# Performance work log

Measured on AMD Instinct MI355X. Metric: run time of the kernel, lower is better.

Reference implementation:

```python
import jax, jax.numpy as jnp
import numpy as np

B = 1024      # number of subgraphs in the batch
S = 128       # nodes per subgraph (last node is the anchor)
N = B * S     # total nodes
E = 2_097_152 # total edges (avg degree 16)
F_IN = 300
F_OUT = 64


def setup_inputs() -> dict:
    key = jax.random.key(0)
    kx, kg, ks, kd, kw = jax.random.split(key, 5)
    in_feat = jax.random.normal(kx, (N, F_IN), dtype=jnp.float32)
    # edges constrained within subgraphs (batched DGL graph semantics)
    gid = jax.random.randint(kg, (E,), 0, B)
    src = (gid * S + jax.random.randint(ks, (E,), 0, S)).astype(jnp.int32)
    dst = (gid * S + jax.random.randint(kd, (E,), 0, S)).astype(jnp.int32)
    W = jax.random.normal(kw, (F_IN, F_OUT), dtype=jnp.float32) * 0.05
    b = jnp.zeros((F_OUT,), dtype=jnp.float32)
    prelu_a = jnp.float32(0.25)  # nn.PReLU default single parameter
    return {"in_feat": in_feat, "W": W, "b": b, "prelu_a": prelu_a,
            "src": src, "dst": dst}


def reference(in_feat, W, b, prelu_a, src, dst):
    ones = jnp.ones((E,), dtype=jnp.float32)
    deg_out = jnp.clip(jax.ops.segment_sum(ones, src, num_segments=N), 1.0)
    deg_in = jnp.clip(jax.ops.segment_sum(ones, dst, num_segments=N), 1.0)
    # GraphConv norm='both': weight first (in_feats > out_feats), then SpMM
    x = in_feat * jax.lax.rsqrt(deg_out)[:, None]
    h = x @ W                                   # [N, F_OUT]
    agg = jax.ops.segment_sum(h[src], dst, num_segments=N)
    h = agg * jax.lax.rsqrt(deg_in)[:, None] + b
    # PReLU
    h = jnp.where(h > 0, h, prelu_a * h)
    # ragged per-subgraph mean over all nodes except the last (anchor)
    node_idx = jnp.arange(N)
    seg = node_idx // S                          # subgraph id per node
    not_anchor = ((node_idx % S) != (S - 1)).astype(h.dtype)
    pool_sum = jax.ops.segment_sum(h * not_anchor[:, None], seg, num_segments=B)
    subgraph_pool_emb = pool_sum / jnp.float32(S - 1)
    anchor_out = h[(jnp.arange(B) + 1) * S - 1]  # last node of each subgraph
    return subgraph_pool_emb, anchor_out
```

## Files before the change

### kernel.cpp

```cpp
#include <hip/hip_runtime.h>
#include <hip/hip_bf16.h>

#define NNODES 131072
#define NEDGES 2097152
#define BSUB   1024
#define SSUB   128
#define FIN    300
#define FOUT   64
#define NCHUNK 256
#define CHEDGE 8192

typedef __attribute__((ext_vector_type(8))) short short8;
typedef __attribute__((ext_vector_type(8))) unsigned short ushort8;
typedef __attribute__((ext_vector_type(4))) float f32x4;

__device__ inline unsigned short f2bfbits(float f) {
    union { __hip_bfloat16 h; unsigned short u; } cv;
    cv.h = __float2bfloat16(f);
    return cv.u;
}
__device__ inline float bf2f(unsigned short b) {
    return __uint_as_float(((unsigned)b) << 16);
}

__device__ inline void gload_lds16(const float* g, void* l) {
    __builtin_amdgcn_global_load_lds(
        (const __attribute__((address_space(1))) unsigned int*)g,
        (__attribute__((address_space(3))) unsigned int*)l,
        16, 0, 0);
}

__global__ __launch_bounds__(256) void prep_w_kernel(const float* __restrict__ W,
                                                     short* __restrict__ wfrag) {
    int idx = blockIdx.x * 256 + threadIdx.x;
    if (idx >= 2560) return;
    int ct   = idx / 640;
    int rem  = idx % 640;
    int kt   = rem / 64;
    int lane = rem % 64;
    int col  = ct * 16 + (lane & 15);
    int kb   = kt * 32 + (lane >> 4) * 8;
#pragma unroll
    for (int e = 0; e < 8; ++e) {
        int k = kb + e;
        float v = (k < FIN) ? W[(size_t)k * FOUT + col] : 0.f;
        wfrag[(size_t)idx * 8 + e] = (short)f2bfbits(v);
    }
}

__global__ __launch_bounds__(256) void bucket_kernel(const int* __restrict__ src,
                                                     const int* __restrict__ dst,
                                                     unsigned* __restrict__ ofs,
                                                     unsigned short* __restrict__ bkt) {
    __shared__ unsigned short epack[CHEDGE];
    __shared__ unsigned short eg[CHEDGE];
    __shared__ unsigned short sorted[CHEDGE];
    __shared__ int hist[BSUB];
    __shared__ int cur[BSUB];
    __shared__ int wsum[4];

    const int cb = blockIdx.x;
    const int t = threadIdx.x;
    for (int i = t; i < BSUB; i += 256) hist[i] = 0;
    __syncthreads();

    const int4* sp = (const int4*)(src + (size_t)cb * CHEDGE);
    const int4* dp = (const int4*)(dst + (size_t)cb * CHEDGE);
    for (int i = t; i < CHEDGE / 4; i += 256) {
        int4 s4 = sp[i], d4 = dp[i];
#pragma unroll
        for (int k = 0; k < 4; ++k) {
            int s = (k == 0) ? s4.x : (k == 1) ? s4.y : (k == 2) ? s4.z : s4.w;
            int d = (k == 0) ? d4.x : (k == 1) ? d4.y : (k == 2) ? d4.z : d4.w;
            int g = s >> 7;
            epack[i * 4 + k] = (unsigned short)(((s & 127) << 7) | (d & 127));
            eg[i * 4 + k] = (unsigned short)g;
            atomicAdd(&hist[g], 1);
        }
    }
    __syncthreads();

    {
        int lane = t & 63, w = t >> 6;
        int c0 = hist[4 * t], c1 = hist[4 * t + 1], c2 = hist[4 * t + 2], c3 = hist[4 * t + 3];
        int s = c0 + c1 + c2 + c3;
        int pre = s;
#pragma unroll
        for (int o = 1; o < 64; o <<= 1) {
            int v = __shfl_up(pre, o, 64);
            if (lane >= o) pre += v;
        }
        if (lane == 63) wsum[w] = pre;
        __syncthreads();
        int wbase = 0;
        for (int i = 0; i < w; ++i) wbase += wsum[i];
        int excl = wbase + pre - s;
        uint4 ov;
        ov.x = ((unsigned)excl << 16) | (unsigned)c0; cur[4 * t]     = excl; excl += c0;
        ov.y = ((unsigned)excl << 16) | (unsigned)c1; cur[4 * t + 1] = excl; excl += c1;
        ov.z = ((unsigned)excl << 16) | (unsigned)c2; cur[4 * t + 2] = excl; excl += c2;
        ov.w = ((unsigned)excl << 16) | (unsigned)c3; cur[4 * t + 3] = excl;
        ((uint4*)(ofs + (size_t)cb * BSUB))[t] = ov;
    }
    __syncthreads();

    for (int i = t; i < CHEDGE; i += 256) {
        int g = eg[i];
        int r = atomicAdd(&cur[g], 1);
        sorted[r] = epack[i];
    }
    __syncthreads();

    {
        ushort8* outv = (ushort8*)(bkt + (size_t)cb * CHEDGE);
        const ushort8* sv = (const ushort8*)sorted;
        for (int i = t; i < CHEDGE / 8; i += 256) outv[i] = sv[i];
    }
}

__global__ __launch_bounds__(256, 2) void gemm_kernel(const float* __restrict__ x,
                                                      const short* __restrict__ wfrag,
                                                      unsigned short* __restrict__ hb) {
    __shared__ __align__(16) char smem[77824];
    char* bufA = smem;
    char* bufB = smem + 32768;
    char* aux  = smem + 65536;

    const int wave = threadIdx.x >> 6;
    const int lane = threadIdx.x & 63;
    const int rowbase = blockIdx.x * 64;

    short8 bq[10];
#pragma unroll
    for (int kt = 0; kt < 10; ++kt)
        bq[kt] = *(const short8*)(wfrag + ((size_t)(wave * 10 + kt) * 64 + lane) * 8);

#pragma unroll
    for (int i = wave; i < 32; i += 4) {
        int o = i * 1024 + lane * 16;
        int row = o >> 9;
        int c = o & 511;
        int csrc = c ^ ((row & 7) << 4);
        gload_lds16(x + (size_t)(rowbase + row) * FIN + (csrc >> 2), bufA + i * 1024);
    }
#pragma unroll
    for (int i = wave; i < 32; i += 4) {
        int o = i * 1024 + lane * 16;
        int row = o >> 9;
        int c = o & 511;
        int csrc = c ^ ((row & 7) << 4);
        gload_lds16(x + (size_t)(rowbase + row) * FIN + 128 + (csrc >> 2), bufB + i * 1024);
    }
    for (int i = wave; i < 11; i += 4) {
        int o = i * 1024 + lane * 16;
        int row = o / 176;
        int c = o - row * 176;
        gload_lds16(x + (size_t)(rowbase + row) * FIN + 256 + (c >> 2), aux + i * 1024);
    }
    ((float*)(aux + 11264))[threadIdx.x] = 0.f;

    f32x4 acc[4];
#pragma unroll
    for (int r = 0; r < 4; ++r) acc[r] = (f32x4){0.f, 0.f, 0.f, 0.f};

    const int kg = lane >> 4;

    __syncthreads();

#pragma unroll
    for (int rt = 0; rt < 4; ++rt) {
        const int rl = rt * 16 + (lane & 15);
        const int sw = (rl & 7) << 4;
#pragma unroll
        for (int kt = 0; kt < 10; ++kt) {
            f32x4 lo, hi;
            if (kt < 8) {
                const char* buf = (kt < 4) ? bufA : bufB;
                int c0 = (kt & 3) * 128 + kg * 32;
                lo = *(const f32x4*)(buf + rl * 512 + (c0 ^ sw));
                hi = *(const f32x4*)(buf + rl * 512 + ((c0 + 16) ^ sw));
            } else {
                int c0 = (kt - 8) * 128 + kg * 32;
                lo = *(const f32x4*)(aux + rl * 176 + c0);
                hi = *(const f32x4*)(aux + rl * 176 + c0 + 16);
            }
            short8 afr;
            afr[0] = (short)f2bfbits(lo[0]); afr[1] = (short)f2bfbits(lo[1]);
            afr[2] = (short)f2bfbits(lo[2]); afr[3] = (short)f2bfbits(lo[3]);
            afr[4] = (short)f2bfbits(hi[0]); afr[5] = (short)f2bfbits(hi[1]);
            afr[6] = (short)f2bfbits(hi[2]); afr[7] = (short)f2bfbits(hi[3]);
            acc[rt] = __builtin_amdgcn_mfma_f32_16x16x32_bf16(afr, bq[kt], acc[rt], 0, 0, 0);
        }
    }

    __syncthreads();

    {
        unsigned short* st = (unsigned short*)aux;
        const int colb = wave * 16 + (lane & 15);
#pragma unroll
        for (int rt = 0; rt < 4; ++rt) {
            const int rbase = rt * 16 + (lane >> 4) * 4;
#pragma unroll
            for (int r = 0; r < 4; ++r)
                st[(rbase + r) * FOUT + colb] = f2bfbits(acc[rt][r]);
        }
        __syncthreads();
        const ushort8* sv = (const ushort8*)st;
        ushort8* hout = (ushort8*)(hb + (size_t)rowbase * FOUT);
        hout[threadIdx.x] = sv[threadIdx.x];
        hout[threadIdx.x + 256] = sv[threadIdx.x + 256];
    }
}

__global__ __launch_bounds__(256) void agg_pool_kernel(const unsigned short* __restrict__ hb,
                                                       const unsigned short* __restrict__ bkt,
                                                       const unsigned* __restrict__ ofs,
                                                       const float* __restrict__ bias,
                                                       const float* __restrict__ prelu,
                                                       float* __restrict__ out) {
    __shared__ unsigned short hl[SSUB][FOUT];
    __shared__ unsigned char  es[SSUB][64];
    __shared__ int   din[SSUB];
    __shared__ int   dout[SSUB];
    __shared__ float rout[SSUB];
    __shared__ float ps[4][FOUT];

    const int g = blockIdx.x;
    const int t = threadIdx.x;
    const int lane = t & 63;
    const int w = t >> 6;

    {
        const ushort8* hsrc = (const ushort8*)(hb + (size_t)g * SSUB * FOUT);
        ushort8* hdst = (ushort8*)&hl[0][0];
        for (int i = t; i < 1024; i += 256) hdst[i] = hsrc[i];
    }
    if (t < SSUB) { din[t] = 0; dout[t] = 0; }
    __syncthreads();

    {
        unsigned w32 = ofs[(size_t)t * BSUB + g];
        int st = (int)(w32 >> 16), cn = (int)(w32 & 0xffff);
        const unsigned short* ebb = bkt + ((size_t)t << 13) + st;
        for (int i = 0; i < cn; ++i) {
            unsigned e = ebb[i];
            int s = e >> 7, d = e & 127;
            int r = atomicAdd(&din[d], 1);
            es[d][r & 63] = (unsigned char)s;
            atomicAdd(&dout[s], 1);
        }
    }
    __syncthreads();
    if (t < SSUB) rout[t] = rsqrtf((float)max(dout[t], 1));
    __syncthreads();

    const float bv = bias[lane];
    const float a = prelu[0];
    float pool = 0.f;
#pragma unroll 4
    for (int ii = 0; ii < 32; ++ii) {
        int d = w + 4 * ii;
        int cd = min(din[d], 64);
        float accv = 0.f;
        const unsigned* ew = (const unsigned*)&es[d][0];
        int nw = (cd + 3) >> 2;
        for (int p = 0; p < nw; ++p) {
            unsigned wd = ew[p];
            int rem = cd - p * 4;
#pragma unroll
            for (int b = 0; b < 4; ++b) {
                if (b < rem) {
                    int s = (wd >> (8 * b)) & 127;
                    accv += bf2f(hl[s][lane]) * rout[s];
                }
            }
        }
        float v = accv * rsqrtf((float)max(din[d], 1)) + bv;
        v = (v > 0.f) ? v : a * v;
        if (d == SSUB - 1)
            out[(size_t)(BSUB + g) * FOUT + lane] = v;
        else
            pool += v;
    }
    ps[w][lane] = pool;
    __syncthreads();
    if (w == 0) {
        float s = (ps[0][lane] + ps[1][lane]) + (ps[2][lane] + ps[3][lane]);
        out[(size_t)g * FOUT + lane] = s * (1.0f / 127.0f);
    }
}

extern "C" void kernel_launch(void* const* d_in, const int* in_sizes, int n_in,
                              void* d_out, int out_size, void* d_ws, size_t ws_size,
                              hipStream_t stream) {
    const float* in_feat = (const float*)d_in[0];
    const float* W       = (const float*)d_in[1];
    const float* bias    = (const float*)d_in[2];
    const float* prelu   = (const float*)d_in[3];
    const int*   src     = (const int*)d_in[4];
    const int*   dst     = (const int*)d_in[5];
    float* out = (float*)d_out;

    char* ws = (char*)d_ws;
    short*          wfrag = (short*)(ws + 65536);
    unsigned*       ofs   = (unsigned*)(ws + (2u << 20));
    unsigned short* bkt   = (unsigned short*)(ws + (4u << 20));
    unsigned short* hb    = (unsigned short*)(ws + (16u << 20));

    hipLaunchKernelGGL(prep_w_kernel,   dim3(10),        dim3(256), 0, stream, W, wfrag);
    hipLaunchKernelGGL(bucket_kernel,   dim3(NCHUNK),    dim3(256), 0, stream, src, dst, ofs, bkt);
    hipLaunchKernelGGL(gemm_kernel,     dim3(NNODES/64), dim3(256), 0, stream, in_feat, wfrag, hb);
    hipLaunchKernelGGL(agg_pool_kernel, dim3(BSUB),      dim3(256), 0, stream, hb, bkt, ofs, bias, prelu, out);
}
```

Measured before the change: 108.0 us.

## Fuse GEMM into per-subgraph aggregation kernel and drop W prep kernel

Merges the dense projection into the aggregation/pooling kernel so each block computes h for its 128 nodes directly into LDS. This removes the bf16 h round-trip through global memory and two kernel launches. W fragments are built per block straight from global memory, and the K tail is loaded into registers instead of LDS. The trade-off is a grid of only 1024 blocks doing the GEMM, which leaves less parallelism and latency hiding than the earlier 2048-block GEMM. Each block also repeats the W conversion.

```diff
diff --git a/kernel.cpp b/kernel.cpp
--- a/kernel.cpp
+++ b/kernel.cpp
@@ -22,30 +22,11 @@
 __device__ inline float bf2f(unsigned short b) {
     return __uint_as_float(((unsigned)b) << 16);
 }
-
 __device__ inline void gload_lds16(const float* g, void* l) {
     __builtin_amdgcn_global_load_lds(
         (const __attribute__((address_space(1))) unsigned int*)g,
         (__attribute__((address_space(3))) unsigned int*)l,
         16, 0, 0);
-}
-
-__global__ __launch_bounds__(256) void prep_w_kernel(const float* __restrict__ W,
-                                                     short* __restrict__ wfrag) {
-    int idx = blockIdx.x * 256 + threadIdx.x;
-    if (idx >= 2560) return;
-    int ct   = idx / 640;
-    int rem  = idx % 640;
-    int kt   = rem / 64;
-    int lane = rem % 64;
-    int col  = ct * 16 + (lane & 15);
-    int kb   = kt * 32 + (lane >> 4) * 8;
-#pragma unroll
-    for (int e = 0; e < 8; ++e) {
-        int k = kb + e;
-        float v = (k < FIN) ? W[(size_t)k * FOUT + col] : 0.f;
-        wfrag[(size_t)idx * 8 + e] = (short)f2bfbits(v);
-    }
 }
 
 __global__ __launch_bounds__(256) void bucket_kernel(const int* __restrict__ src,
@@ -118,126 +99,139 @@
     }
 }
 
-__global__ __launch_bounds__(256, 2) void gemm_kernel(const float* __restrict__ x,
-                                                      const short* __restrict__ wfrag,
-                                                      unsigned short* __restrict__ hb) {
-    __shared__ __align__(16) char smem[77824];
-    char* bufA = smem;
-    char* bufB = smem + 32768;
-    char* aux  = smem + 65536;
-
-    const int wave = threadIdx.x >> 6;
-    const int lane = threadIdx.x & 63;
-    const int rowbase = blockIdx.x * 64;
-
-    short8 bq[10];
-#pragma unroll
-    for (int kt = 0; kt < 10; ++kt)
-        bq[kt] = *(const short8*)(wfrag + ((size_t)(wave * 10 + kt) * 64 + lane) * 8);
-
-#pragma unroll
-    for (int i = wave; i < 32; i += 4) {
-        int o = i * 1024 + lane * 16;
-        int row = o >> 9;
-        int c = o & 511;
-        int csrc = c ^ ((row & 7) << 4);
-        gload_lds16(x + (size_t)(rowbase + row) * FIN + (csrc >> 2), bufA + i * 1024);
-    }
-#pragma unroll
-    for (int i = wave; i < 32; i += 4) {
-        int o = i * 1024 + lane * 16;
-        int row = o >> 9;
-        int c = o & 511;
-        int csrc = c ^ ((row & 7) << 4);
-        gload_lds16(x + (size_t)(rowbase + row) * FIN + 128 + (csrc >> 2), bufB + i * 1024);
-    }
-    for (int i = wave; i < 11; i += 4) {
-        int o = i * 1024 + lane * 16;
-        int row = o / 176;
-        int c = o - row * 176;
-        gload_lds16(x + (size_t)(rowbase + row) * FIN + 256 + (c >> 2), aux + i * 1024);
-    }
-    ((float*)(aux + 11264))[threadIdx.x] = 0.f;
-
-    f32x4 acc[4];
-#pragma unroll
-    for (int r = 0; r < 4; ++r) acc[r] = (f32x4){0.f, 0.f, 0.f, 0.f};
-
-    const int kg = lane >> 4;
-
-    __syncthreads();
-
-#pragma unroll
-    for (int rt = 0; rt < 4; ++rt) {
-        const int rl = rt * 16 + (lane & 15);
-        const int sw = (rl & 7) << 4;
-#pragma unroll
-        for (int kt = 0; kt < 10; ++kt) {
-            f32x4 lo, hi;
-            if (kt < 8) {
-                const char* buf = (kt < 4) ? bufA : bufB;
-                int c0 = (kt & 3) * 128 + kg * 32;
-                lo = *(const f32x4*)(buf + rl * 512 + (c0 ^ sw));
-                hi = *(const f32x4*)(buf + rl * 512 + ((c0 + 16) ^ sw));
-            } else {
-                int c0 = (kt - 8) * 128 + kg * 32;
-                lo = *(const f32x4*)(aux + rl * 176 + c0);
-                hi = *(const f32x4*)(aux + rl * 176 + c0 + 16);
-            }
-            short8 afr;
-            afr[0] = (short)f2bfbits(lo[0]); afr[1] = (short)f2bfbits(lo[1]);
-            afr[2] = (short)f2bfbits(lo[2]); afr[3] = (short)f2bfbits(lo[3]);
-            afr[4] = (short)f2bfbits(hi[0]); afr[5] = (short)f2bfbits(hi[1]);
-            afr[6] = (short)f2bfbits(hi[2]); afr[7] = (short)f2bfbits(hi[3]);
-            acc[rt] = __builtin_amdgcn_mfma_f32_16x16x32_bf16(afr, bq[kt], acc[rt], 0, 0, 0);
-        }
-    }
-
-    __syncthreads();
-
-    {
-        unsigned short* st = (unsigned short*)aux;
-        const int colb = wave * 16 + (lane & 15);
-#pragma unroll
-        for (int rt = 0; rt < 4; ++rt) {
-            const int rbase = rt * 16 + (lane >> 4) * 4;
-#pragma unroll
-            for (int r = 0; r < 4; ++r)
-                st[(rbase + r) * FOUT + colb] = f2bfbits(acc[rt][r]);
-        }
-        __syncthreads();
-        const ushort8* sv = (const ushort8*)st;
-        ushort8* hout = (ushort8*)(hb + (size_t)rowbase * FOUT);
-        hout[threadIdx.x] = sv[threadIdx.x];
-        hout[threadIdx.x + 256] = sv[threadIdx.x + 256];
-    }
-}
-
-__global__ __launch_bounds__(256) void agg_pool_kernel(const unsigned short* __restrict__ hb,
+__global__ __launch_bounds__(256, 2) void fused_kernel(const float* __restrict__ x,
+                                                       const float* __restrict__ W,
                                                        const unsigned short* __restrict__ bkt,
                                                        const unsigned* __restrict__ ofs,
                                                        const float* __restrict__ bias,
                                                        const float* __restrict__ prelu,
                                                        float* __restrict__ out) {
-    __shared__ unsigned short hl[SSUB][FOUT];
-    __shared__ unsigned char  es[SSUB][64];
-    __shared__ int   din[SSUB];
-    __shared__ int   dout[SSUB];
-    __shared__ float rout[SSUB];
-    __shared__ float ps[4][FOUT];
+    __shared__ __align__(16) char smem[59904];
+    char*           buf  = smem;
+    unsigned short* hl   = (unsigned short*)(smem + 32768);
+    unsigned char*  es   = (unsigned char*)(smem + 49152);
+    int*            din  = (int*)(smem + 57344);
+    int*            dout = (int*)(smem + 57856);
+    float*          rout = (float*)(smem + 58368);
+    float*          ps   = (float*)(smem + 58880);
 
     const int g = blockIdx.x;
     const int t = threadIdx.x;
     const int lane = t & 63;
-    const int w = t >> 6;
-
+    const int wave = t >> 6;
+    const int kg = lane >> 4;
+
+    short8 bq[10];
     {
-        const ushort8* hsrc = (const ushort8*)(hb + (size_t)g * SSUB * FOUT);
-        ushort8* hdst = (ushort8*)&hl[0][0];
-        for (int i = t; i < 1024; i += 256) hdst[i] = hsrc[i];
+        const int colW = wave * 16 + (lane & 15);
+        const int krow = kg * 8;
+#pragma unroll
+        for (int kt = 0; kt < 10; ++kt) {
+#pragma unroll
+            for (int e = 0; e < 8; ++e) {
+                int k = kt * 32 + krow + e;
+                float v = (k < FIN) ? W[(size_t)k * FOUT + colW] : 0.f;
+                bq[kt][e] = (short)f2bfbits(v);
+            }
+        }
     }
     if (t < SSUB) { din[t] = 0; dout[t] = 0; }
-    __syncthreads();
+
+#pragma unroll
+    for (int half = 0; half < 2; ++half) {
+        const int rowbase = g * SSUB + half * 64;
+
+        f32x4 t8l[4], t8h[4], t9l[4], t9h[4];
+#pragma unroll
+        for (int rt = 0; rt < 4; ++rt) {
+            const float* arp = x + (size_t)(rowbase + rt * 16 + (lane & 15)) * FIN;
+            t8l[rt] = *(const f32x4*)(arp + 256 + kg * 8);
+            t8h[rt] = *(const f32x4*)(arp + 256 + kg * 8 + 4);
+            t9l[rt] = (f32x4){0.f, 0.f, 0.f, 0.f};
+            t9h[rt] = (f32x4){0.f, 0.f, 0.f, 0.f};
+            if (kg == 0) {
+                t9l[rt] = *(const f32x4*)(arp + 288);
+                t9h[rt] = *(const f32x4*)(arp + 292);
+            } else if (kg == 1) {
+                t9l[rt] = *(const f32x4*)(arp + 296);
+            }
+        }
+
+#pragma unroll
+        for (int i = wave; i < 32; i += 4) {
+            int o = i * 1024 + lane * 16;
+            int row = o >> 9;
+            int c = o & 511;
+            int csrc = c ^ ((row & 7) << 4);
+            gload_lds16(x + (size_t)(rowbase + row) * FIN + (csrc >> 2), buf + i * 1024);
+        }
+
+        f32x4 acc[4];
+#pragma unroll
+        for (int r = 0; r < 4; ++r) acc[r] = (f32x4){0.f, 0.f, 0.f, 0.f};
+
+        __syncthreads();
+
+#pragma unroll
+        for (int rt = 0; rt < 4; ++rt) {
+            const int rl = rt * 16 + (lane & 15);
+            const int sw = (rl & 7) << 4;
+#pragma unroll
+            for (int kt = 0; kt < 4; ++kt) {
+                int c0 = kt * 128 + kg * 32;
+                f32x4 lo = *(const f32x4*)(buf + rl * 512 + (c0 ^ sw));
+                f32x4 hi = *(const f32x4*)(buf + rl * 512 + ((c0 + 16) ^ sw));
+                short8 afr;
+                afr[0] = (short)f2bfbits(lo[0]); afr[1] = (short)f2bfbits(lo[1]);
+                afr[2] = (short)f2bfbits(lo[2]); afr[3] = (short)f2bfbits(lo[3]);
+                afr[4] = (short)f2bfbits(hi[0]); afr[5] = (short)f2bfbits(hi[1]);
+                afr[6] = (short)f2bfbits(hi[2]); afr[7] = (short)f2bfbits(hi[3]);
+                acc[rt] = __builtin_amdgcn_mfma_f32_16x16x32_bf16(afr, bq[kt], acc[rt], 0, 0, 0);
+            }
+        }
+        __syncthreads();
+
+#pragma unroll
+        for (int i = wave; i < 32; i += 4) {
+            int o = i * 1024 + lane * 16;
+            int row = o >> 9;
+            int c = o & 511;
+            int csrc = c ^ ((row & 7) << 4);
+            gload_lds16(x + (size_t)(rowbase + row) * FIN + 128 + (csrc >> 2), buf + i * 1024);
+        }
+        __syncthreads();
+
+#pragma unroll
+        for (int rt = 0; rt < 4; ++rt) {
+            const int rl = rt * 16 + (lane & 15);
+            const int sw = (rl & 7) << 4;
+#pragma unroll
+            for (int kt = 4; kt < 10; ++kt) {
+                f32x4 lo, hi;
+                if (kt < 8) {
+                    int c0 = (kt - 4) * 128 + kg * 32;
+                    lo = *(const f32x4*)(buf + rl * 512 + (c0 ^ sw));
+                    hi = *(const f32x4*)(buf + rl * 512 + ((c0 + 16) ^ sw));
+                } else if (kt == 8) {
+                    lo = t8l[rt]; hi = t8h[rt];
+                } else {
+                    lo = t9l[rt]; hi = t9h[rt];
+                }
+                short8 afr;
+                afr[0] = (short)f2bfbits(lo[0]); afr[1] = (short)f2bfbits(lo[1]);
+                afr[2] = (short)f2bfbits(lo[2]); afr[3] = (short)f2bfbits(lo[3]);
+                afr[4] = (short)f2bfbits(hi[0]); afr[5] = (short)f2bfbits(hi[1]);
+                afr[6] = (short)f2bfbits(hi[2]); afr[7] = (short)f2bfbits(hi[3]);
+                acc[rt] = __builtin_amdgcn_mfma_f32_16x16x32_bf16(afr, bq[kt], acc[rt], 0, 0, 0);
+            }
+            const int colb = wave * 16 + (lane & 15);
+            const int rbase = half * 64 + rt * 16 + (lane >> 4) * 4;
+#pragma unroll
+            for (int r = 0; r < 4; ++r)
+                hl[(rbase + r) * FOUT + colb] = f2bfbits(acc[rt][r]);
+        }
+        __syncthreads();
+    }
 
     {
         unsigned w32 = ofs[(size_t)t * BSUB + g];
@@ -247,7 +241,7 @@
             unsigned e = ebb[i];
             int s = e >> 7, d = e & 127;
             int r = atomicAdd(&din[d], 1);
-            es[d][r & 63] = (unsigned char)s;
+            es[d * 64 + (r & 63)] = (unsigned char)s;
             atomicAdd(&dout[s], 1);
         }
     }
@@ -260,10 +254,10 @@
     float pool = 0.f;
 #pragma unroll 4
     for (int ii = 0; ii < 32; ++ii) {
-        int d = w + 4 * ii;
+        int d = wave + 4 * ii;
         int cd = min(din[d], 64);
         float accv = 0.f;
-        const unsigned* ew = (const unsigned*)&es[d][0];
+        const unsigned* ew = (const unsigned*)&es[d * 64];
         int nw = (cd + 3) >> 2;
         for (int p = 0; p < nw; ++p) {
             unsigned wd = ew[p];
@@ -272,7 +266,7 @@
             for (int b = 0; b < 4; ++b) {
                 if (b < rem) {
                     int s = (wd >> (8 * b)) & 127;
-                    accv += bf2f(hl[s][lane]) * rout[s];
+                    accv += bf2f(hl[s * FOUT + lane]) * rout[s];
                 }
             }
         }
@@ -283,10 +277,10 @@
         else
             pool += v;
     }
-    ps[w][lane] = pool;
-    __syncthreads();
-    if (w == 0) {
-        float s = (ps[0][lane] + ps[1][lane]) + (ps[2][lane] + ps[3][lane]);
+    ps[wave * 64 + lane] = pool;
+    __syncthreads();
+    if (wave == 0) {
+        float s = (ps[lane] + ps[64 + lane]) + (ps[128 + lane] + ps[192 + lane]);
         out[(size_t)g * FOUT + lane] = s * (1.0f / 127.0f);
     }
 }
@@ -303,13 +297,11 @@
     float* out = (float*)d_out;
 
     char* ws = (char*)d_ws;
-    short*          wfrag = (short*)(ws + 65536);
-    unsigned*       ofs   = (unsigned*)(ws + (2u << 20));
-    unsigned short* bkt   = (unsigned short*)(ws + (4u << 20));
-    unsigned short* hb    = (unsigned short*)(ws + (16u << 20));
-
-    hipLaunchKernelGGL(prep_w_kernel,   dim3(10),        dim3(256), 0, stream, W, wfrag);
-    hipLaunchKernelGGL(bucket_kernel,   dim3(NCHUNK),    dim3(256), 0, stream, src, dst, ofs, bkt);
-    hipLaunchKernelGGL(gemm_kernel,     dim3(NNODES/64), dim3(256), 0, stream, in_feat, wfrag, hb);
-    hipLaunchKernelGGL(agg_pool_kernel, dim3(BSUB),      dim3(256), 0, stream, hb, bkt, ofs, bias, prelu, out);
-}
+    unsigned*       ofs = (unsigned*)(ws + (2u << 20));
+    unsigned short* bkt = (unsigned short*)(ws + (4u << 20));
+
+    hipLaunchKernelGGL(bucket_kernel, dim3(NCHUNK), dim3(256), 0, stream,
+                       src, dst, ofs, bkt);
+    hipLaunchKernelGGL(fused_kernel,  dim3(BSUB),   dim3(256), 0, stream,
+                       in_feat, W, bkt, ofs, bias, prelu, out);
+}
```

Measured after the change: 140.3 us. 1.3x slower.
